# Kernel optimization log

Measured on AMD Instinct MI355X. Metric: run time of the kernel, lower is better.

The kernel has to match this reference:

```python
import jax, jax.numpy as jnp
import numpy as np

B, T, D_MODEL = 4, 2048, 2048
H, D, R = 16, 128, 512


def apply_rope(x, cos, sin):
    # x: [B,H,T,D]; cos/sin: [T, D//2] -> interleave-duplicated to [1,1,T,D]
    x1 = x[..., ::2]
    x2 = x[..., 1::2]
    x_rot = jnp.stack([-x2, x1], axis=-1).reshape(x.shape)
    cos_e = jnp.repeat(cos, 2, axis=-1)[None, None]  # [1,1,T,D]
    sin_e = jnp.repeat(sin, 2, axis=-1)[None, None]
    return x * cos_e + x_rot * sin_e


def setup_inputs() -> dict:
    key = jax.random.key(0)
    ks = jax.random.split(key, 6)
    scale = 0.02
    x = jax.random.normal(ks[0], (B, T, D_MODEL), jnp.float32)
    # standard RoPE frequencies
    pos = jnp.arange(T, dtype=jnp.float32)
    inv_freq = 1.0 / (10000.0 ** (jnp.arange(0, D, 2, dtype=jnp.float32) / D))
    ang = pos[:, None] * inv_freq[None, :]  # [T, D//2]
    cos = jnp.cos(ang)
    sin = jnp.sin(ang)
    Wq = jax.random.normal(ks[1], (D_MODEL, H * D), jnp.float32) * scale
    Wkd = jax.random.normal(ks[2], (D_MODEL, R), jnp.float32) * scale
    Wku = jax.random.normal(ks[3], (R, 2 * H * D), jnp.float32) * scale
    Wo = jax.random.normal(ks[4], (H * D, D_MODEL), jnp.float32) * scale
    return {"x": x, "cos": cos, "sin": sin, "Wq": Wq, "Wkd": Wkd, "Wku": Wku, "Wo": Wo}


def reference(x, cos, sin, Wq, Wkd, Wku, Wo):
    # q projection: [B,T,H*D] -> [B,H,T,D]
    q = (x @ Wq).reshape(B, T, H, D).transpose(0, 2, 1, 3)
    # low-rank KV: down to rank R, up to 2*H*D
    kv_lat = x @ Wkd                     # [B,T,R]
    kv = (kv_lat @ Wku).reshape(B, T, 2, H, D)
    k = kv[:, :, 0].transpose(0, 2, 1, 3)  # [B,H,T,D]
    v = kv[:, :, 1].transpose(0, 2, 1, 3)
    q = apply_rope(q, cos, sin)
    k = apply_rope(k, cos, sin)
    # causal SDPA
    scores = jnp.einsum("bhtd,bhsd->bhts", q, k) / jnp.sqrt(jnp.float32(D))
    causal = jnp.tril(jnp.ones((T, T), dtype=bool))
    scores = jnp.where(causal[None, None], scores, jnp.finfo(scores.dtype).min)
    probs = jax.nn.softmax(scores, axis=-1)
    out = jnp.einsum("bhts,bhsd->bhtd", probs, v)
    out = out.transpose(0, 2, 1, 3).reshape(B, T, H * D)
    return out @ Wo
```

## Files before the change

### kernel.cpp

```cpp
#include <hip/hip_runtime.h>

typedef __bf16 bf16x8 __attribute__((ext_vector_type(8)));
typedef float  f32x4  __attribute__((ext_vector_type(4)));
typedef float  f32x16 __attribute__((ext_vector_type(16)));
typedef unsigned int u32;
typedef unsigned int u32x4 __attribute__((ext_vector_type(4)));
typedef unsigned short u16;

#define LOG2E    1.4426950408889634f
#define SM_SCALE 0.08838834764831845f

__device__ __forceinline__ u16 f2bf(float f) {
    unsigned int u = __builtin_bit_cast(unsigned int, f);
    u += 0x7fffu + ((u >> 16) & 1u);
    return (u16)(u >> 16);
}
__device__ __forceinline__ float b2f(u16 h) {
    unsigned int u = ((unsigned int)h) << 16;
    return __builtin_bit_cast(float, u);
}
__device__ __forceinline__ void glds16(const void* g, void* l) {
    __builtin_amdgcn_global_load_lds(
        (__attribute__((address_space(1))) void*)g,
        (__attribute__((address_space(3))) void*)l, 16, 0, 0);
}

__global__ void cvt_bf16_k(const float* __restrict__ in, u16* __restrict__ out, size_t n4) {
    size_t i = (size_t)blockIdx.x * blockDim.x + threadIdx.x;
    size_t stride = (size_t)gridDim.x * blockDim.x;
    for (; i < n4; i += stride) {
        float4 v = ((const float4*)in)[i];
        ushort4 r;
        r.x = f2bf(v.x); r.y = f2bf(v.y); r.z = f2bf(v.z); r.w = f2bf(v.w);
        ((ushort4*)out)[i] = r;
    }
}

__global__ void transpose_w_k(const float* __restrict__ W, u16* __restrict__ WT, int K, int N) {
    __shared__ float tile[32][33];
    int tx = threadIdx.x & 31, ty = threadIdx.x >> 5;
    int bx = blockIdx.x, by = blockIdx.y;
    #pragma unroll
    for (int i = 0; i < 4; ++i) {
        int r = by*32 + ty + i*8;
        tile[ty + i*8][tx] = W[(size_t)r * N + bx*32 + tx];
    }
    __syncthreads();
    #pragma unroll
    for (int i = 0; i < 4; ++i) {
        int n = bx*32 + ty + i*8;
        WT[(size_t)n * K + by*32 + tx] = f2bf(tile[tx][ty + i*8]);
    }
}

__global__ void transpose_v_k(const u16* __restrict__ V, u16* __restrict__ VT) {
    __shared__ u16 tile[32][33];
    int tx = threadIdx.x & 31, ty = threadIdx.x >> 5;
    int tT = blockIdx.x, tD = blockIdx.y, bh = blockIdx.z;
    int b = bh >> 4, h = bh & 15;
    #pragma unroll
    for (int i = 0; i < 4; ++i) {
        int t = tT*32 + ty + i*8;
        int d = tD*32 + tx;
        tile[ty + i*8][tx] = V[((size_t)(b*2048 + t))*2048 + h*128 + d];
    }
    __syncthreads();
    #pragma unroll
    for (int i = 0; i < 4; ++i) {
        int d = tD*32 + ty + i*8;
        int t = tT*32 + tx;
        VT[((size_t)bh*128 + d)*2048 + t] = tile[tx][ty + i*8];
    }
}

__global__ void rope_k(u16* __restrict__ X, const float* __restrict__ C, const float* __restrict__ S,
                       float scale) {
    size_t idx = (size_t)blockIdx.x * blockDim.x + threadIdx.x;
    size_t pair0 = idx * 4;
    int i = (int)(pair0 & 63);
    size_t rem = pair0 >> 6;
    int t = (int)((rem >> 4) & 2047);
    float4 cv = *(const float4*)(C + (size_t)t*64 + i);
    float4 sv = *(const float4*)(S + (size_t)t*64 + i);
    ushort4 lo = ((const ushort4*)X)[idx*2];
    ushort4 hi = ((const ushort4*)X)[idx*2 + 1];
    float e0 = b2f(lo.x), o0 = b2f(lo.y), e1 = b2f(lo.z), o1 = b2f(lo.w);
    float e2 = b2f(hi.x), o2 = b2f(hi.y), e3 = b2f(hi.z), o3 = b2f(hi.w);
    ushort4 r0, r1;
    r0.x = f2bf((e0*cv.x - o0*sv.x)*scale); r0.y = f2bf((o0*cv.x + e0*sv.x)*scale);
    r0.z = f2bf((e1*cv.y - o1*sv.y)*scale); r0.w = f2bf((o1*cv.y + e1*sv.y)*scale);
    r1.x = f2bf((e2*cv.z - o2*sv.z)*scale); r1.y = f2bf((o2*cv.z + e2*sv.z)*scale);
    r1.z = f2bf((e3*cv.w - o3*sv.w)*scale); r1.w = f2bf((o3*cv.w + e3*sv.w)*scale);
    ((ushort4*)X)[idx*2]     = r0;
    ((ushort4*)X)[idx*2 + 1] = r1;
}

template<int MODE>
__global__ void gemm_bt_k(const u16* __restrict__ A, const u16* __restrict__ BT,
                          void* __restrict__ O0, void* __restrict__ O1, int N, int K)
{
    __shared__ alignas(16) u16 As[128*64];
    __shared__ alignas(16) u16 Bs[128*64];
    const int tid  = threadIdx.x;
    const int wave = tid >> 6, lane = tid & 63;
    const int l15 = lane & 15, l4 = lane >> 4;
    const int wm = wave >> 1, wn = wave & 1;
    const size_t arow0 = (size_t)blockIdx.x * 128;
    const size_t brow0 = (size_t)blockIdx.y * 128;
    const u16* Ab = A  + arow0 * K;
    const u16* Bb = BT + brow0 * K;

    f32x4 acc[4][4] = {};

    for (int k0 = 0; k0 < K; k0 += 64) {
        #pragma unroll
        for (int j = 0; j < 4; ++j) {
            int p = j*256 + wave*64 + lane;
            int row = p >> 3, slot = p & 7;
            int gs = slot ^ (row & 7);
            glds16(Ab + (size_t)row*K + k0 + gs*8, &As[(size_t)(j*256 + wave*64)*8]);
            glds16(Bb + (size_t)row*K + k0 + gs*8, &Bs[(size_t)(j*256 + wave*64)*8]);
        }
        __syncthreads();
        #pragma unroll
        for (int kk = 0; kk < 2; ++kk) {
            bf16x8 af[4], bfr[4];
            #pragma unroll
            for (int m = 0; m < 4; ++m) {
                int row = wm*64 + m*16 + l15;
                int byt = row*128 + (((kk*4 + l4)*16) ^ ((row & 7) << 4));
                af[m] = *(const bf16x8*)&As[byt >> 1];
            }
            #pragma unroll
            for (int n = 0; n < 4; ++n) {
                int row = wn*64 + n*16 + l15;
                int byt = row*128 + (((kk*4 + l4)*16) ^ ((row & 7) << 4));
                bfr[n] = *(const bf16x8*)&Bs[byt >> 1];
            }
            #pragma unroll
            for (int m = 0; m < 4; ++m)
                #pragma unroll
                for (int n = 0; n < 4; ++n)
                    acc[m][n] = __builtin_amdgcn_mfma_f32_16x16x32_bf16(af[m], bfr[n], acc[m][n], 0, 0, 0);
        }
        __syncthreads();
    }

    #pragma unroll
    for (int m = 0; m < 4; ++m)
      #pragma unroll
      for (int n = 0; n < 4; ++n)
        #pragma unroll
        for (int j = 0; j < 4; ++j) {
            size_t row = arow0 + wm*64 + m*16 + l4*4 + j;
            size_t col = brow0 + wn*64 + n*16 + l15;
            float v = acc[m][n][j];
            if (MODE == 0) {
                ((u16*)O0)[row * N + col] = f2bf(v);
            } else if (MODE == 1) {
                ((float*)O0)[row * N + col] = v;
            } else {
                if (col < 2048) ((u16*)O0)[row * 2048 + col]          = f2bf(v);
                else            ((u16*)O1)[row * 2048 + (col - 2048)] = f2bf(v);
            }
        }
}

__global__ __launch_bounds__(256, 2) void attn_k(const u16* __restrict__ Qg, const u16* __restrict__ Kg,
                       const u16* __restrict__ VTg, u16* __restrict__ Og)
{
    __shared__ alignas(16) u16 Ks[2][64*128];
    __shared__ alignas(16) u16 Vs[2][128*64];
    const int tid = threadIdx.x, wave = tid >> 6, lane = tid & 63;
    const int l31 = lane & 31, hi = lane >> 5;

    int flat = blockIdx.x + 16*blockIdx.y;
    int nf = (flat & 7)*128 + (flat >> 3);
    const int qt = 15 - (nf & 15), bh = nf >> 4;
    const int b = bh >> 4, h = bh & 15;
    const u16* kb_ = Kg  + ((size_t)b*2048)*2048 + h*128;
    const u16* vtb = VTg + (size_t)bh*128*2048;
    const int q0 = qt*128, wq0 = q0 + wave*32, qv = wq0 + l31;

    bf16x8 qf[8];
    {
        const u16* qb = Qg + ((size_t)(b*2048 + qv))*2048 + h*128;
        #pragma unroll
        for (int kst = 0; kst < 8; ++kst)
            qf[kst] = *(const bf16x8*)(qb + kst*16 + hi*8);
    }

    f32x16 oacc[4] = {};
    float mrun = -__builtin_inff(), lrun = 0.f;

    auto STAGE = [&](int bi, int kb) {
        #pragma unroll
        for (int j = 0; j < 4; ++j) {
            int p = j*256 + wave*64 + lane;
            { int row = p >> 4, slot = p & 15, gs = slot ^ (row & 7);
              glds16(kb_ + (size_t)(kb + row)*2048 + gs*8, &Ks[bi][(j*256 + wave*64)*8]); }
            { int row = p >> 3, slot = p & 7,  gs = slot ^ (row & 7);
              glds16(vtb + (size_t)row*2048 + kb + gs*8,   &Vs[bi][(j*256 + wave*64)*8]); }
        }
    };

    const int NT = 2*qt + 2;
    STAGE(0, 0);
    __syncthreads();

    for (int it = 0; it < NT; ++it) {
        const int cur = it & 1;
        const int kb0 = it * 64;
        if (it + 1 < NT) STAGE(cur ^ 1, (it + 1) * 64);

        if (kb0 <= wq0 + 31) {
            f32x16 s[2];
            #pragma unroll
            for (int t = 0; t < 2; ++t) {
                f32x16 sa = {};
                #pragma unroll
                for (int kst = 0; kst < 8; ++kst) {
                    int row = t*32 + l31;
                    int ch = (kst*2 + hi) ^ (row & 7);
                    bf16x8 kf = *(const bf16x8*)&Ks[cur][row*128 + ch*8];
                    sa = __builtin_amdgcn_mfma_f32_32x32x16_bf16(kf, qf[kst], sa, 0, 0, 0);
                }
                s[t] = sa;
            }
            if (kb0 + 63 > wq0) {
                #pragma unroll
                for (int t = 0; t < 2; ++t)
                    #pragma unroll
                    for (int r = 0; r < 16; ++r) {
                        int key = kb0 + t*32 + (r & 3) + 8*(r >> 2) + 4*hi;
                        if (key > qv) s[t][r] = -__builtin_inff();
                    }
            }
            float pm = s[0][0];
            #pragma unroll
            for (int r = 1; r < 16; ++r) pm = fmaxf(pm, s[0][r]);
            #pragma unroll
            for (int r = 0; r < 16; ++r) pm = fmaxf(pm, s[1][r]);
            pm = fmaxf(pm, __shfl_xor(pm, 32));
            if (!__all(pm <= mrun + 8.0f)) {
                float mnew = fmaxf(mrun, pm);
                float alpha = exp2f(mrun - mnew);
                mrun = mnew;
                lrun *= alpha;
                #pragma unroll
                for (int dt = 0; dt < 4; ++dt)
                    #pragma unroll
                    for (int r = 0; r < 16; ++r) oacc[dt][r] *= alpha;
            }
            float sum = 0.f;
            #pragma unroll
            for (int t = 0; t < 2; ++t)
                #pragma unroll
                for (int r = 0; r < 16; ++r) {
                    float p = exp2f(s[t][r] - mrun);
                    s[t][r] = p;
                    sum += p;
                }
            sum += __shfl_xor(sum, 32);
            lrun += sum;
            u32 P2[2][4][2];
            #pragma unroll
            for (int t = 0; t < 2; ++t)
                #pragma unroll
                for (int g = 0; g < 4; ++g)
                    #pragma unroll
                    for (int i = 0; i < 2; ++i)
                        asm("v_cvt_pk_bf16_f32 %0, %1, %2"
                            : "=v"(P2[t][g][i])
                            : "v"(s[t][g*4 + 2*i]), "v"(s[t][g*4 + 2*i + 1]));
            #pragma unroll
            for (int kst = 0; kst < 4; ++kst) {
                const int t = kst >> 1, bg = (kst & 1)*2;
                u32 own0 = hi ? P2[t][bg+1][0] : P2[t][bg][0];
                u32 own1 = hi ? P2[t][bg+1][1] : P2[t][bg][1];
                u32 snd0 = hi ? P2[t][bg][0]   : P2[t][bg+1][0];
                u32 snd1 = hi ? P2[t][bg][1]   : P2[t][bg+1][1];
                u32 rcv0 = (u32)__shfl_xor((int)snd0, 32);
                u32 rcv1 = (u32)__shfl_xor((int)snd1, 32);
                u32x4 wv;
                wv.x = hi ? rcv0 : own0;
                wv.y = hi ? rcv1 : own1;
                wv.z = hi ? own0 : rcv0;
                wv.w = hi ? own1 : rcv1;
                bf16x8 pf = __builtin_bit_cast(bf16x8, wv);
                #pragma unroll
                for (int dt = 0; dt < 4; ++dt) {
                    int row = dt*32 + l31;
                    int ch = (kst*2 + hi) ^ (row & 7);
                    bf16x8 vf = *(const bf16x8*)&Vs[cur][row*64 + ch*8];
                    oacc[dt] = __builtin_amdgcn_mfma_f32_32x32x16_bf16(vf, pf, oacc[dt], 0, 0, 0);
                }
            }
        }
        __syncthreads();
    }

    float inv = 1.0f / lrun;
    u16* ob = Og + ((size_t)(b*2048 + qv))*2048 + h*128;
    #pragma unroll
    for (int dt = 0; dt < 4; ++dt)
        #pragma unroll
        for (int rg = 0; rg < 4; ++rg) {
            float a0 = oacc[dt][rg*4+0]*inv, a1 = oacc[dt][rg*4+1]*inv;
            float a2 = oacc[dt][rg*4+2]*inv, a3 = oacc[dt][rg*4+3]*inv;
            u32 wA, wB;
            asm("v_cvt_pk_bf16_f32 %0, %1, %2" : "=v"(wA) : "v"(a0), "v"(a1));
            asm("v_cvt_pk_bf16_f32 %0, %1, %2" : "=v"(wB) : "v"(a2), "v"(a3));
            int dbase = dt*32 + rg*8 + hi*4;
            *(u32*)(ob + dbase)     = wA;
            *(u32*)(ob + dbase + 2) = wB;
        }
}

extern "C" void kernel_launch(void* const* d_in, const int* in_sizes, int n_in,
                              void* d_out, int out_size, void* d_ws, size_t ws_size,
                              hipStream_t stream)
{
    const float* x    = (const float*)d_in[0];
    const float* cosT = (const float*)d_in[1];
    const float* sinT = (const float*)d_in[2];
    const float* Wq   = (const float*)d_in[3];
    const float* Wkd  = (const float*)d_in[4];
    const float* Wku  = (const float*)d_in[5];
    const float* Wo   = (const float*)d_in[6];
    float* out = (float*)d_out;

    char* p = (char*)d_ws;
    u16* buf0  = (u16*)p; p += (size_t)16777216*2;
    u16* WqT   = (u16*)p; p += (size_t) 4194304*2;
    u16* WkdT  = (u16*)p; p += (size_t) 1048576*2;
    u16* WkuT  = (u16*)p; p += (size_t) 2097152*2;
    u16* WoT   = (u16*)p; p += (size_t) 4194304*2;
    u16* qbuf  = (u16*)p; p += (size_t)16777216*2;
    u16* kbuf  = (u16*)p; p += (size_t)16777216*2;
    u16* vtb   = (u16*)p; p += (size_t)16777216*2;
    u16* kvlat = (u16*)p; p += (size_t) 4194304*2;

    cvt_bf16_k<<<4096, 256, 0, stream>>>(x, buf0, (size_t)4194304);

    transpose_w_k<<<dim3(  64, 64), 256, 0, stream>>>(Wq,  WqT,  2048, 2048);
    transpose_w_k<<<dim3(  16, 64), 256, 0, stream>>>(Wkd, WkdT, 2048,  512);
    transpose_w_k<<<dim3( 128, 16), 256, 0, stream>>>(Wku, WkuT,  512, 4096);
    transpose_w_k<<<dim3(  64, 64), 256, 0, stream>>>(Wo,  WoT,  2048, 2048);

    gemm_bt_k<0><<<dim3(64, 16), 256, 0, stream>>>(buf0,  WqT,  qbuf,  nullptr, 2048, 2048);
    gemm_bt_k<0><<<dim3(64,  4), 256, 0, stream>>>(buf0,  WkdT, kvlat, nullptr,  512, 2048);
    gemm_bt_k<2><<<dim3(64, 32), 256, 0, stream>>>(kvlat, WkuT, kbuf,  buf0,    4096,  512);

    rope_k<<<8192, 256, 0, stream>>>(qbuf, cosT, sinT, SM_SCALE * LOG2E);
    rope_k<<<8192, 256, 0, stream>>>(kbuf, cosT, sinT, 1.0f);

    transpose_v_k<<<dim3(64, 4, 64), 256, 0, stream>>>(buf0, vtb);

    attn_k<<<dim3(16, 64), 256, 0, stream>>>(qbuf, kbuf, vtb, buf0);

    gemm_bt_k<1><<<dim3(64, 16), 256, 0, stream>>>(buf0, WoT, out, nullptr, 2048, 2048);
}
```

Baseline: 553.7 us.

## Shrink attention KV tile, raise occupancy, remap workgroups, add MFMA priority

The attention kernel now streams K/V in 32-key tiles instead of 64, which halves LDS use and lets launch bounds target four workgroups per CU. It also remaps blocks so each XCD handles whole (batch, head) groups, which should improve K/V L2 reuse. The GEMM kernel gets an XCD-aware tile swizzle that hardcodes 64 tiles along x, and both kernels raise wave priority around MFMA bursts. Smaller tiles mean more iterations and barriers. The attention remap also drops the longest-first ordering of query tiles, which can hurt load balance under the causal mask.

```diff
diff --git a/kernel.cpp b/kernel.cpp
--- a/kernel.cpp
+++ b/kernel.cpp
@@ -105,8 +105,15 @@
     const int wave = tid >> 6, lane = tid & 63;
     const int l15 = lane & 15, l4 = lane >> 4;
     const int wm = wave >> 1, wn = wave & 1;
-    const size_t arow0 = (size_t)blockIdx.x * 128;
-    const size_t brow0 = (size_t)blockIdx.y * 128;
+
+    const int nwg = gridDim.x * gridDim.y;
+    int f = blockIdx.x + gridDim.x * blockIdx.y;
+    f = (f & 7) * (nwg >> 3) + (f >> 3);
+    const int bx = f & 63;
+    const int by = f >> 6;
+
+    const size_t arow0 = (size_t)bx * 128;
+    const size_t brow0 = (size_t)by * 128;
     const u16* Ab = A  + arow0 * K;
     const u16* Bb = BT + brow0 * K;
 
@@ -137,11 +144,13 @@
                 int byt = row*128 + (((kk*4 + l4)*16) ^ ((row & 7) << 4));
                 bfr[n] = *(const bf16x8*)&Bs[byt >> 1];
             }
+            __builtin_amdgcn_s_setprio(1);
             #pragma unroll
             for (int m = 0; m < 4; ++m)
                 #pragma unroll
                 for (int n = 0; n < 4; ++n)
                     acc[m][n] = __builtin_amdgcn_mfma_f32_16x16x32_bf16(af[m], bfr[n], acc[m][n], 0, 0, 0);
+            __builtin_amdgcn_s_setprio(0);
         }
         __syncthreads();
     }
@@ -166,17 +175,17 @@
         }
 }
 
-__global__ __launch_bounds__(256, 2) void attn_k(const u16* __restrict__ Qg, const u16* __restrict__ Kg,
+__global__ __launch_bounds__(256, 4) void attn_k(const u16* __restrict__ Qg, const u16* __restrict__ Kg,
                        const u16* __restrict__ VTg, u16* __restrict__ Og)
 {
-    __shared__ alignas(16) u16 Ks[2][64*128];
-    __shared__ alignas(16) u16 Vs[2][128*64];
+    __shared__ alignas(16) u16 Ks[2][32*128];
+    __shared__ alignas(16) u16 Vs[2][128*32];
     const int tid = threadIdx.x, wave = tid >> 6, lane = tid & 63;
     const int l31 = lane & 31, hi = lane >> 5;
 
-    int flat = blockIdx.x + 16*blockIdx.y;
-    int nf = (flat & 7)*128 + (flat >> 3);
-    const int qt = 15 - (nf & 15), bh = nf >> 4;
+    int f = blockIdx.x + 16*blockIdx.y;
+    const int xcd = f & 7, w = f >> 3;
+    const int bh = xcd*8 + (w >> 4), qt = w & 15;
     const int b = bh >> 4, h = bh & 15;
     const u16* kb_ = Kg  + ((size_t)b*2048)*2048 + h*128;
     const u16* vtb = VTg + (size_t)bh*128*2048;
@@ -195,52 +204,44 @@
 
     auto STAGE = [&](int bi, int kb) {
         #pragma unroll
-        for (int j = 0; j < 4; ++j) {
+        for (int j = 0; j < 2; ++j) {
             int p = j*256 + wave*64 + lane;
             { int row = p >> 4, slot = p & 15, gs = slot ^ (row & 7);
               glds16(kb_ + (size_t)(kb + row)*2048 + gs*8, &Ks[bi][(j*256 + wave*64)*8]); }
-            { int row = p >> 3, slot = p & 7,  gs = slot ^ (row & 7);
-              glds16(vtb + (size_t)row*2048 + kb + gs*8,   &Vs[bi][(j*256 + wave*64)*8]); }
+            { int d = p >> 2, slot = p & 3, gs = slot ^ (d & 3);
+              glds16(vtb + (size_t)d*2048 + kb + gs*8,     &Vs[bi][(j*256 + wave*64)*8]); }
         }
     };
 
-    const int NT = 2*qt + 2;
+    const int NT = 4*qt + 4;
     STAGE(0, 0);
     __syncthreads();
 
     for (int it = 0; it < NT; ++it) {
         const int cur = it & 1;
-        const int kb0 = it * 64;
-        if (it + 1 < NT) STAGE(cur ^ 1, (it + 1) * 64);
+        const int kb0 = it * 32;
+        if (it + 1 < NT) STAGE(cur ^ 1, kb0 + 32);
 
         if (kb0 <= wq0 + 31) {
-            f32x16 s[2];
-            #pragma unroll
-            for (int t = 0; t < 2; ++t) {
-                f32x16 sa = {};
-                #pragma unroll
-                for (int kst = 0; kst < 8; ++kst) {
-                    int row = t*32 + l31;
-                    int ch = (kst*2 + hi) ^ (row & 7);
-                    bf16x8 kf = *(const bf16x8*)&Ks[cur][row*128 + ch*8];
-                    sa = __builtin_amdgcn_mfma_f32_32x32x16_bf16(kf, qf[kst], sa, 0, 0, 0);
+            f32x16 s = {};
+            __builtin_amdgcn_s_setprio(1);
+            #pragma unroll
+            for (int kst = 0; kst < 8; ++kst) {
+                int ch = (kst*2 + hi) ^ (l31 & 7);
+                bf16x8 kf = *(const bf16x8*)&Ks[cur][l31*128 + ch*8];
+                s = __builtin_amdgcn_mfma_f32_32x32x16_bf16(kf, qf[kst], s, 0, 0, 0);
+            }
+            __builtin_amdgcn_s_setprio(0);
+            if (kb0 == wq0) {
+                #pragma unroll
+                for (int r = 0; r < 16; ++r) {
+                    int key = kb0 + (r & 3) + 8*(r >> 2) + 4*hi;
+                    if (key > qv) s[r] = -__builtin_inff();
                 }
-                s[t] = sa;
-            }
-            if (kb0 + 63 > wq0) {
-                #pragma unroll
-                for (int t = 0; t < 2; ++t)
-                    #pragma unroll
-                    for (int r = 0; r < 16; ++r) {
-                        int key = kb0 + t*32 + (r & 3) + 8*(r >> 2) + 4*hi;
-                        if (key > qv) s[t][r] = -__builtin_inff();
-                    }
-            }
-            float pm = s[0][0];
-            #pragma unroll
-            for (int r = 1; r < 16; ++r) pm = fmaxf(pm, s[0][r]);
-            #pragma unroll
-            for (int r = 0; r < 16; ++r) pm = fmaxf(pm, s[1][r]);
+            }
+            float pm = s[0];
+            #pragma unroll
+            for (int r = 1; r < 16; ++r) pm = fmaxf(pm, s[r]);
             pm = fmaxf(pm, __shfl_xor(pm, 32));
             if (!__all(pm <= mrun + 8.0f)) {
                 float mnew = fmaxf(mrun, pm);
@@ -254,47 +255,42 @@
             }
             float sum = 0.f;
             #pragma unroll
-            for (int t = 0; t < 2; ++t)
-                #pragma unroll
-                for (int r = 0; r < 16; ++r) {
-                    float p = exp2f(s[t][r] - mrun);
-                    s[t][r] = p;
-                    sum += p;
-                }
+            for (int r = 0; r < 16; ++r) {
+                float p = exp2f(s[r] - mrun);
+                s[r] = p;
+                sum += p;
+            }
             sum += __shfl_xor(sum, 32);
             lrun += sum;
-            u32 P2[2][4][2];
-            #pragma unroll
-            for (int t = 0; t < 2; ++t)
-                #pragma unroll
-                for (int g = 0; g < 4; ++g)
-                    #pragma unroll
-                    for (int i = 0; i < 2; ++i)
-                        asm("v_cvt_pk_bf16_f32 %0, %1, %2"
-                            : "=v"(P2[t][g][i])
-                            : "v"(s[t][g*4 + 2*i]), "v"(s[t][g*4 + 2*i + 1]));
-            #pragma unroll
-            for (int kst = 0; kst < 4; ++kst) {
-                const int t = kst >> 1, bg = (kst & 1)*2;
-                u32 own0 = hi ? P2[t][bg+1][0] : P2[t][bg][0];
-                u32 own1 = hi ? P2[t][bg+1][1] : P2[t][bg][1];
-                u32 snd0 = hi ? P2[t][bg][0]   : P2[t][bg+1][0];
-                u32 snd1 = hi ? P2[t][bg][1]   : P2[t][bg+1][1];
-                u32 rcv0 = (u32)__shfl_xor((int)snd0, 32);
-                u32 rcv1 = (u32)__shfl_xor((int)snd1, 32);
+            u32 P2[4][2];
+            #pragma unroll
+            for (int g = 0; g < 4; ++g)
+                #pragma unroll
+                for (int i = 0; i < 2; ++i)
+                    asm("v_cvt_pk_bf16_f32 %0, %1, %2"
+                        : "=v"(P2[g][i])
+                        : "v"(s[g*4 + 2*i]), "v"(s[g*4 + 2*i + 1]));
+            #pragma unroll
+            for (int kst = 0; kst < 2; ++kst) {
+                const int go = 2*kst + hi, gs_ = 2*kst + 1 - hi;
+                u32 own0 = P2[go][0],  own1 = P2[go][1];
+                u32 rcv0 = (u32)__shfl_xor((int)P2[gs_][0], 32);
+                u32 rcv1 = (u32)__shfl_xor((int)P2[gs_][1], 32);
                 u32x4 wv;
                 wv.x = hi ? rcv0 : own0;
                 wv.y = hi ? rcv1 : own1;
                 wv.z = hi ? own0 : rcv0;
                 wv.w = hi ? own1 : rcv1;
                 bf16x8 pf = __builtin_bit_cast(bf16x8, wv);
+                __builtin_amdgcn_s_setprio(1);
                 #pragma unroll
                 for (int dt = 0; dt < 4; ++dt) {
-                    int row = dt*32 + l31;
-                    int ch = (kst*2 + hi) ^ (row & 7);
-                    bf16x8 vf = *(const bf16x8*)&Vs[cur][row*64 + ch*8];
+                    int d = dt*32 + l31;
+                    int ch = (kst*2 + hi) ^ (d & 3);
+                    bf16x8 vf = *(const bf16x8*)&Vs[cur][d*32 + ch*8];
                     oacc[dt] = __builtin_amdgcn_mfma_f32_32x32x16_bf16(vf, pf, oacc[dt], 0, 0, 0);
                 }
+                __builtin_amdgcn_s_setprio(0);
             }
         }
         __syncthreads();
@@ -312,8 +308,7 @@
             asm("v_cvt_pk_bf16_f32 %0, %1, %2" : "=v"(wA) : "v"(a0), "v"(a1));
             asm("v_cvt_pk_bf16_f32 %0, %1, %2" : "=v"(wB) : "v"(a2), "v"(a3));
             int dbase = dt*32 + rg*8 + hi*4;
-            *(u32*)(ob + dbase)     = wA;
-            *(u32*)(ob + dbase + 2) = wB;
+            *(uint2*)(ob + dbase) = make_uint2(wA, wB);
         }
 }
 
```

After: 825.2 us. 1.49x slower.
